# Kernel tuning notes

Measured on AMD Instinct MI355X. Metric: run time of the kernel, lower is better.

The kernel has to match this reference:

```python
import jax, jax.numpy as jnp
import numpy as np

EPS = 1e-12  # torch F.normalize eps


def _l2norm(x, axis):
    n = jnp.maximum(jnp.linalg.norm(x, axis=axis, keepdims=True), EPS)
    return x / n


def setup_inputs() -> dict:
    key = jax.random.key(0)
    k1, k2, k3, k4, k5 = jax.random.split(key, 5)
    N, E, IN_DIM, FAC_K, DIM_K = 100000, 1600000, 64, 4, 16
    all_emb = jax.random.normal(k1, (N, IN_DIM), dtype=jnp.float32) * 0.1
    W = jax.random.normal(k2, (FAC_K, IN_DIM, DIM_K), dtype=jnp.float32) * (1.0 / np.sqrt(IN_DIM))
    b = jax.random.normal(k3, (FAC_K, 1, DIM_K), dtype=jnp.float32) * 0.02
    row = jax.random.randint(k4, (E,), 0, N, dtype=jnp.int32)
    col = jax.random.randint(k5, (E,), 0, N, dtype=jnp.int32)
    return {"all_emb": all_emb, "W": W, "b": b, "row": row, "col": col, "iter_k": 2}


def reference(all_emb, W, b, row, col, iter_k):
    N = all_emb.shape[0]
    # factorized projection: [N, in_dim] x [K, in_dim, dk] -> [K, N, dk]
    fac = jnp.einsum('nd,kdf->knf', all_emb, W + b)
    fac = jax.nn.leaky_relu(fac, negative_slope=0.2)
    fac = _l2norm(fac, axis=2)

    new_fac = fac
    for _ in range(iter_k):
        head = new_fac[:, row]            # [K, E, dk]
        tail = fac[:, col]                # [K, E, dk]
        p_uv = jnp.sum(head * tail, axis=2)   # [K, E]
        p_uv = jax.nn.softmax(p_uv, axis=0)   # softmax over factors
        p_uv = jax.lax.stop_gradient(p_uv)    # original detaches attention
        msg = p_uv[:, :, None] * tail         # [K, E, dk]
        agg = jax.vmap(lambda m: jax.ops.segment_sum(m, row, num_segments=N))(msg)
        new_fac = _l2norm(fac + agg, axis=2)  # [K, N, dk]

    # torch.cat(list(new_fac_emb), dim=1) -> [N, K*dk]
    out = jnp.transpose(new_fac, (1, 0, 2)).reshape(N, -1)
    return out
```

## Files before the change

kernel.cpp:

```cpp
#include <hip/hip_runtime.h>

#define IN_DIM 64
#define FAC_K  4
#define DIM_K  16
#define SH     5
#define EPB    8192
#define CAP    1536

typedef _Float16 h2v __attribute__((ext_vector_type(2)));
typedef _Float16 h8v __attribute__((ext_vector_type(8)));
typedef float    f4v __attribute__((ext_vector_type(4)));

__device__ inline int   h2i(h2v v) { return __builtin_bit_cast(int, v); }
__device__ inline h2v   i2h(int v) { return __builtin_bit_cast(h2v, v); }
__device__ inline h2v   pkh(float a, float b) {
    return __builtin_bit_cast(h2v, __builtin_amdgcn_cvt_pkrtz(a, b));
}

#if __has_builtin(__builtin_amdgcn_fdot2)
__device__ inline float FDOT2(h2v a, h2v b, float c) {
    return __builtin_amdgcn_fdot2(a, b, c, false);
}
#else
__device__ inline float FDOT2(h2v a, h2v b, float c) {
    return c + (float)a.x * (float)b.x + (float)a.y * (float)b.y;
}
#endif

__device__ inline float qadd_xor1(float x) {
    int y = __builtin_amdgcn_update_dpp(0, __builtin_bit_cast(int, x), 0xB1, 0xF, 0xF, true);
    return x + __builtin_bit_cast(float, y);
}
__device__ inline float qadd_xor2(float x) {
    int y = __builtin_amdgcn_update_dpp(0, __builtin_bit_cast(int, x), 0x4E, 0xF, 0xF, true);
    return x + __builtin_bit_cast(float, y);
}
__device__ inline int rowxor8_i(int x) {
    return __builtin_amdgcn_update_dpp(0, x, 0x128, 0xF, 0xF, true);
}

union H8U { h8v v; h2v p[4]; };

#define TSZ 1344

__global__ __launch_bounds__(256) void fac_hist_kernel(
    const float* __restrict__ emb, const float* __restrict__ W,
    const float* __restrict__ b,   _Float16* __restrict__ fac16,
    const int* __restrict__ row,   int* __restrict__ H,
    int N, int E, int FB, int NB_blk, int NBUK)
{
    __shared__ float lds_pool[4 * TSZ];
    const int tid = threadIdx.x;

    if (blockIdx.x >= FB) {
        int* hist = (int*)lds_pool;
        const int hb   = blockIdx.x - FB;
        const int base = hb * EPB;
        for (int i = tid; i < NBUK; i += 256) hist[i] = 0;
        __syncthreads();
#pragma unroll
        for (int i = 0; i < EPB / 256; ++i) {
            int e = base + i * 256 + tid;
            if (e < E) atomicAdd(&hist[row[e] >> SH], 1);
        }
        __syncthreads();
        for (int i = tid; i < NBUK; i += 256)
            H[(size_t)i * NB_blk + hb] = hist[i];
        return;
    }

    const int lane = tid & 63;
    const int l    = lane & 15;
    const int q    = lane >> 4;
    float* T = lds_pool + (tid >> 6) * TSZ;

    H8U Bf[4][2];
#pragma unroll
    for (int t = 0; t < 4; ++t) {
        const float bv = b[16 * t + l];
#pragma unroll
        for (int s = 0; s < 2; ++s) {
            const float* wp = W + t * 1024 + (32 * s + 8 * q) * 16 + l;
#pragma unroll
            for (int jp = 0; jp < 4; ++jp) {
                float w0 = wp[(2 * jp)     * 16] + bv;
                float w1 = wp[(2 * jp + 1) * 16] + bv;
                Bf[t][s].p[jp] = pkh(w0, w1);
            }
        }
    }

    const int ntiles = (N + 15) >> 4;
    const int nw     = FB * 4;
    const int wid    = (blockIdx.x * 256 + tid) >> 6;

    for (int tile = wid; tile < ntiles; tile += nw) {
        const int n0 = tile << 4;
        int nm = n0 + l; if (nm >= N) nm = N - 1;

        f4v acc[4];
#pragma unroll
        for (int t = 0; t < 4; ++t) acc[t] = f4v{0.f, 0.f, 0.f, 0.f};

#pragma unroll
        for (int s = 0; s < 2; ++s) {
            const float4* ap = (const float4*)(emb + (size_t)nm * 64 + 32 * s + 8 * q);
            float4 a0 = ap[0], a1 = ap[1];
            H8U A;
            A.p[0] = pkh(a0.x, a0.y); A.p[1] = pkh(a0.z, a0.w);
            A.p[2] = pkh(a1.x, a1.y); A.p[3] = pkh(a1.z, a1.w);
#pragma unroll
            for (int t = 0; t < 4; ++t)
                acc[t] = __builtin_amdgcn_mfma_f32_16x16x32_f16(A.v, Bf[t][s].v, acc[t], 0, 0, 0);
        }

#pragma unroll
        for (int t = 0; t < 4; ++t) {
            f4v v = acc[t];
            f4v vr;
#pragma unroll
            for (int r = 0; r < 4; ++r)
                vr[r] = fmaxf(v[r], 0.f) + 0.2f * fminf(v[r], 0.f);
            const int o = 16 * t + l;
            ((f4v*)(T + 20 * o + 16 * t + 4 * q))[0] = vr;
        }
        float vv[16];
        float ss = 0.f;
#pragma unroll
        for (int i = 0; i < 16; ++i) {
            float x = T[20 * (16 * q + i) + 16 * q + l];
            vv[i] = x;
            ss = fmaf(x, x, ss);
        }
        float inv = 1.0f / fmaxf(sqrtf(ss), 1e-12f);
        H8U o0, o1;
#pragma unroll
        for (int jp = 0; jp < 4; ++jp) {
            o0.p[jp] = pkh(vv[2 * jp]     * inv, vv[2 * jp + 1] * inv);
            o1.p[jp] = pkh(vv[8 + 2 * jp] * inv, vv[9 + 2 * jp] * inv);
        }
        if (n0 + l < N) {
            uint4* dst = (uint4*)(fac16 + (size_t)(n0 + l) * 64 + q * 16);
            dst[0] = __builtin_bit_cast(uint4, o0.v);
            dst[1] = __builtin_bit_cast(uint4, o1.v);
        }
    }
}

__global__ __launch_bounds__(1024) void scan1_kernel(
    const int* __restrict__ in, int* __restrict__ out,
    int* __restrict__ bsum, int M)
{
    __shared__ int wsum[16];
    const int tid  = threadIdx.x;
    const int lane = tid & 63;
    const int w    = tid >> 6;
    const int gi   = blockIdx.x * 1024 + tid;

    int sc = (gi < M) ? in[gi] : 0;
#pragma unroll
    for (int d = 1; d < 64; d <<= 1) {
        int y = __shfl_up(sc, d);
        if (lane >= d) sc += y;
    }
    if (lane == 63) wsum[w] = sc;
    __syncthreads();
    if (w == 0) {
        int v = (lane < 16) ? wsum[lane] : 0;
#pragma unroll
        for (int d = 1; d < 16; d <<= 1) {
            int y = __shfl_up(v, d);
            if (lane >= d) v += y;
        }
        if (lane < 16) wsum[lane] = v;
    }
    __syncthreads();
    if (w > 0) sc += wsum[w - 1];
    if (gi < M) out[gi + 1] = sc;
    if (tid == 1023) bsum[blockIdx.x] = sc;
    if (blockIdx.x == 0 && tid == 0) out[0] = 0;
}

__global__ __launch_bounds__(1024) void scan2_kernel(int* __restrict__ bsum, int nb)
{
    __shared__ int sm[1024];
    const int tid = threadIdx.x;
    sm[tid] = (tid < nb) ? bsum[tid] : 0;
    __syncthreads();
    for (int d = 1; d < 1024; d <<= 1) {
        int t = (tid >= d) ? sm[tid - d] : 0;
        __syncthreads();
        sm[tid] += t;
        __syncthreads();
    }
    if (tid < nb) bsum[tid] = (tid > 0) ? sm[tid - 1] : 0;
}

__global__ __launch_bounds__(256) void scatter1_kernel(
    const int* __restrict__ row, const int* __restrict__ col,
    const int* __restrict__ Hscan, const int* __restrict__ bsum,
    int* __restrict__ tmp, int E, int NB_blk, int NBUK)
{
    __shared__ int cur[3200];
    const int tid = threadIdx.x;
    const int jb  = blockIdx.x;
    const int base = jb * EPB;
    for (int i = tid; i < NBUK; i += 256) {
        int g = i * NB_blk + jb;
        int v = Hscan[g];
        if (g >= 1) v += bsum[(g - 1) >> 10];
        cur[i] = v;
    }
    __syncthreads();
#pragma unroll
    for (int it = 0; it < EPB / 256; ++it) {
        int e = base + it * 256 + tid;
        if (e < E) {
            int r = row[e];
            int pos = atomicAdd(&cur[r >> SH], 1);
            tmp[pos] = ((r & 31) << 24) | (col[e] << 7);
        }
    }
}

__global__ __launch_bounds__(256, 8) void agg_kernel(
    const _Float16* __restrict__ fac16, const int* __restrict__ tmp,
    const int* __restrict__ Hscan, const int* __restrict__ bsum,
    float* __restrict__ nf_out, int E, int NB_blk, int NBUK, int N)
{
    __shared__ int csr[CAP];
    __shared__ int hist[32];
    __shared__ int curx[32];
    __shared__ int offl[33];

    const int tid = threadIdx.x;
    const int b   = blockIdx.x;

    const int g0 = b * NB_blk;
    const int gE = g0 + NB_blk;
    const int start = Hscan[g0] + (g0 >= 1 ? bsum[(g0 - 1) >> 10] : 0);
    const int end   = Hscan[gE] + bsum[(gE - 1) >> 10];
    const int cnt   = end - start;
    const bool fits = (cnt <= CAP);

    if (tid < 32) hist[tid] = 0;
    __syncthreads();
    if (fits) {
        for (int i = tid; i < cnt; i += 256)
            atomicAdd(&hist[tmp[start + i] >> 24], 1);
    }
    __syncthreads();
    if (tid < 32) {
        int e = hist[tid];
        int sc = e;
#pragma unroll
        for (int d = 1; d < 32; d <<= 1) {
            int y = __shfl_up(sc, d);
            if (tid >= d) sc += y;
        }
        int ex = sc - e;
        offl[tid] = ex;
        curx[tid] = ex;
        if (tid == 31) offl[32] = sc;
    }
    __syncthreads();
    if (fits) {
        for (int i = tid; i < cnt; i += 256) {
            int u = tmp[start + i];
            int pos = atomicAdd(&curx[u >> 24], 1);
            csr[pos] = u & 0xFFFFFF;
        }
    }
    __syncthreads();

    const int grp = tid >> 4;
    const int k   = tid & 3;
    const int q   = (tid >> 2) & 3;
    const char* facB = (const char*)fac16;
    const int   kb   = k * 32;

    for (int round = 0; round < 2; ++round) {
        const int lr = round * 16 + grp;
        const int n  = (b << SH) + lr;
        if (n >= N) continue;

        const _Float16* frow = fac16 + (size_t)n * 64 + k * 16;
        uint4 fa = ((const uint4*)frow)[0];
        uint4 fb = ((const uint4*)frow)[1];
        h2v fh[8] = { i2h(fa.x), i2h(fa.y), i2h(fa.z), i2h(fa.w),
                      i2h(fb.x), i2h(fb.y), i2h(fb.z), i2h(fb.w) };
        float f32[16];
#pragma unroll
        for (int r = 0; r < 8; ++r) { f32[2*r] = (float)fh[r].x; f32[2*r+1] = (float)fh[r].y; }
        h2v hh[8];
#pragma unroll
        for (int r = 0; r < 8; ++r) hh[r] = fh[r];

        int s_l = 0, len = 0;
        if (fits) { s_l = offl[lr]; len = offl[lr + 1] - s_l; }

        float vv[16];
#pragma unroll 1
        for (int pass = 0; pass < 2; ++pass) {
            h2v acc2[8];
#pragma unroll
            for (int r = 0; r < 8; ++r) acc2[r] = h2v{(_Float16)0.f, (_Float16)0.f};

            if (fits) {
                if (len > 0) {
                    int e0 = (q < len) ? q : len - 1;
                    const uint4* tp0 = (const uint4*)(facB + csr[s_l + e0] + kb);
                    uint4 ta0 = tp0[0], tb0 = tp0[1];
                    uint4 ta1 = ta0, tb1 = tb0;
                    if (len > 4) {
                        int e1 = (4 + q < len) ? 4 + q : len - 1;
                        const uint4* tp1 = (const uint4*)(facB + csr[s_l + e1] + kb);
                        ta1 = tp1[0]; tb1 = tp1[1];
                    }
                    for (int i = 0; i < len; i += 4) {
                        uint4 a = ta0, bb2 = tb0;
                        ta0 = ta1; tb0 = tb1;
                        const bool valid = (i + q) < len;
                        if (i + 8 < len) {
                            int e2 = (i + 8 + q < len) ? i + 8 + q : len - 1;
                            const uint4* tp2 = (const uint4*)(facB + csr[s_l + e2] + kb);
                            ta1 = tp2[0]; tb1 = tp2[1];
                        }
                        h2v t2[8] = { i2h(a.x), i2h(a.y), i2h(a.z), i2h(a.w),
                                      i2h(bb2.x), i2h(bb2.y), i2h(bb2.z), i2h(bb2.w) };
                        float p = 0.f;
#pragma unroll
                        for (int r = 0; r < 8; ++r) p = FDOT2(hh[r], t2[r], p);
                        float exv = valid ? __expf(p) : 0.f;
                        float qs = qadd_xor1(exv);
                        qs = qadd_xor2(qs);
                        float w = valid ? exv * __builtin_amdgcn_rcpf(qs) : 0.f;
                        _Float16 wh = (_Float16)w;
                        h2v w2; w2.x = wh; w2.y = wh;
#pragma unroll
                        for (int r = 0; r < 8; ++r) acc2[r] += w2 * t2[r];
                    }
                }
            } else {
                for (int i = 0; i < cnt; ++i) {
                    int u = tmp[start + i];
                    if ((u >> 24) != lr) continue;
                    const uint4* tp = (const uint4*)(facB + (u & 0xFFFFFF) + kb);
                    uint4 a = tp[0], bb2 = tp[1];
                    h2v t2[8] = { i2h(a.x), i2h(a.y), i2h(a.z), i2h(a.w),
                                  i2h(bb2.x), i2h(bb2.y), i2h(bb2.z), i2h(bb2.w) };
                    float p = 0.f;
#pragma unroll
                    for (int r = 0; r < 8; ++r) p = FDOT2(hh[r], t2[r], p);
                    float exv = __expf(p);
                    float qs = qadd_xor1(exv);
                    qs = qadd_xor2(qs);
                    float w = (q == 0) ? exv * __builtin_amdgcn_rcpf(qs) : 0.f;
                    _Float16 wh = (_Float16)w;
                    h2v w2; w2.x = wh; w2.y = wh;
#pragma unroll
                    for (int r = 0; r < 8; ++r) acc2[r] += w2 * t2[r];
                }
            }

#pragma unroll
            for (int r = 0; r < 8; ++r) {
                acc2[r] += i2h(__shfl_xor(h2i(acc2[r]), 4));
                acc2[r] += i2h(rowxor8_i(h2i(acc2[r])));
            }
            float ss = 0.f;
#pragma unroll
            for (int r = 0; r < 8; ++r) {
                vv[2*r]   = f32[2*r]   + (float)acc2[r].x;
                vv[2*r+1] = f32[2*r+1] + (float)acc2[r].y;
            }
#pragma unroll
            for (int d = 0; d < 16; ++d) ss = fmaf(vv[d], vv[d], ss);
            float inv = 1.0f / fmaxf(sqrtf(ss), 1e-12f);
#pragma unroll
            for (int d = 0; d < 16; ++d) vv[d] *= inv;
            if (pass == 0) {
#pragma unroll
                for (int r = 0; r < 8; ++r) {
                    h2v t; t.x = (_Float16)vv[2*r]; t.y = (_Float16)vv[2*r+1];
                    hh[r] = t;
                }
            }
        }

        float4 o;
        o.x = (q==0) ? vv[0]  : (q==1) ? vv[4]  : (q==2) ? vv[8]  : vv[12];
        o.y = (q==0) ? vv[1]  : (q==1) ? vv[5]  : (q==2) ? vv[9]  : vv[13];
        o.z = (q==0) ? vv[2]  : (q==1) ? vv[6]  : (q==2) ? vv[10] : vv[14];
        o.w = (q==0) ? vv[3]  : (q==1) ? vv[7]  : (q==2) ? vv[11] : vv[15];
        ((float4*)(nf_out + (size_t)n * 64 + k * 16))[q] = o;
    }
}

extern "C" void kernel_launch(void* const* d_in, const int* in_sizes, int n_in,
                              void* d_out, int out_size, void* d_ws, size_t ws_size,
                              hipStream_t stream) {
    const float* emb = (const float*)d_in[0];
    const float* W   = (const float*)d_in[1];
    const float* b   = (const float*)d_in[2];
    const int*   row = (const int*)d_in[3];
    const int*   col = (const int*)d_in[4];

    const int N = in_sizes[0] / IN_DIM;
    const int E = in_sizes[3];

    const int NBUK   = (N + 31) >> SH;
    const int NB_blk = (E + EPB - 1) / EPB;
    const int M      = NBUK * NB_blk;

    float* nf = (float*)d_out;

    _Float16* fac16 = (_Float16*)d_ws;
    int*      tmp   = (int*)(fac16 + (size_t)N * 64);
    int*      H     = tmp + E;
    int*      Hscan = H + M;
    int*      bsum  = Hscan + (M + 1);

    const int nb1 = (M + 1023) / 1024;
    const int FB  = 512;

    fac_hist_kernel<<<FB + NB_blk, 256, 0, stream>>>(
        emb, W, b, fac16, row, H, N, E, FB, NB_blk, NBUK);
    scan1_kernel<<<nb1, 1024, 0, stream>>>(H, Hscan, bsum, M);
    scan2_kernel<<<1, 1024, 0, stream>>>(bsum, nb1);
    scatter1_kernel<<<NB_blk, 256, 0, stream>>>(row, col, Hscan, bsum, tmp, E, NB_blk, NBUK);
    agg_kernel<<<NBUK, 256, 0, stream>>>(fac16, tmp, Hscan, bsum, nf, E, NB_blk, NBUK, N);
}
```

Before: 210.6 us.

## Replace per-block histogram scan with global bucket counts and atomic scatter

The per-(bucket, block) histogram matrix and its two-level scan are replaced by a single global per-bucket histogram built with global atomics, a one-block scan, and a scatter that claims positions through padded global atomic cursors. The aggregation kernel becomes persistent, with 2048 blocks pulling buckets from an atomic ticket counter. This cuts scan work and kernel launches, but adds contention on global atomics during the scatter and changes the order of edges inside each bucket, which also makes the fp16 accumulation order nondeterministic. The scan kernel handles at most 4096 buckets, which covers the 3125 buckets this input needs.

```diff
diff --git a/kernel.cpp b/kernel.cpp
--- a/kernel.cpp
+++ b/kernel.cpp
@@ -4,8 +4,8 @@
 #define FAC_K  4
 #define DIM_K  16
 #define SH     5
-#define EPB    8192
 #define CAP    1536
+#define HB     64
 
 typedef _Float16 h2v __attribute__((ext_vector_type(2)));
 typedef _Float16 h8v __attribute__((ext_vector_type(8)));
@@ -41,31 +41,35 @@
 
 union H8U { h8v v; h2v p[4]; };
 
+__global__ __launch_bounds__(256) void zero_kernel(int* __restrict__ p, int n)
+{
+    int i = blockIdx.x * 256 + threadIdx.x;
+    if (i < n) p[i] = 0;
+}
+
 #define TSZ 1344
 
 __global__ __launch_bounds__(256) void fac_hist_kernel(
     const float* __restrict__ emb, const float* __restrict__ W,
     const float* __restrict__ b,   _Float16* __restrict__ fac16,
-    const int* __restrict__ row,   int* __restrict__ H,
-    int N, int E, int FB, int NB_blk, int NBUK)
+    const int* __restrict__ row,   int* __restrict__ Hglob,
+    int N, int E, int FB, int NBUK)
 {
     __shared__ float lds_pool[4 * TSZ];
     const int tid = threadIdx.x;
 
     if (blockIdx.x >= FB) {
         int* hist = (int*)lds_pool;
-        const int hb   = blockIdx.x - FB;
-        const int base = hb * EPB;
+        const int hb = blockIdx.x - FB;
         for (int i = tid; i < NBUK; i += 256) hist[i] = 0;
         __syncthreads();
-#pragma unroll
-        for (int i = 0; i < EPB / 256; ++i) {
-            int e = base + i * 256 + tid;
-            if (e < E) atomicAdd(&hist[row[e] >> SH], 1);
-        }
-        __syncthreads();
-        for (int i = tid; i < NBUK; i += 256)
-            H[(size_t)i * NB_blk + hb] = hist[i];
+        for (int e = hb * 256 + tid; e < E; e += HB * 256)
+            atomicAdd(&hist[row[e] >> SH], 1);
+        __syncthreads();
+        for (int i = tid; i < NBUK; i += 256) {
+            int v = hist[i];
+            if (v) atomicAdd(&Hglob[i], v);
+        }
         return;
     }
 
@@ -147,17 +151,23 @@
     }
 }
 
-__global__ __launch_bounds__(1024) void scan1_kernel(
-    const int* __restrict__ in, int* __restrict__ out,
-    int* __restrict__ bsum, int M)
+__global__ __launch_bounds__(1024) void scan_kernel(
+    const int* __restrict__ Hglob, int* __restrict__ Hstart,
+    int* __restrict__ curp, int NBUK, int E)
 {
     __shared__ int wsum[16];
     const int tid  = threadIdx.x;
     const int lane = tid & 63;
     const int w    = tid >> 6;
-    const int gi   = blockIdx.x * 1024 + tid;
-
-    int sc = (gi < M) ? in[gi] : 0;
+    const int base = tid * 4;
+
+    int v[4]; int tot = 0;
+#pragma unroll
+    for (int j = 0; j < 4; ++j) {
+        v[j] = (base + j < NBUK) ? Hglob[base + j] : 0;
+        tot += v[j];
+    }
+    int sc = tot;
 #pragma unroll
     for (int d = 1; d < 64; d <<= 1) {
         int y = __shfl_up(sc, d);
@@ -166,234 +176,214 @@
     if (lane == 63) wsum[w] = sc;
     __syncthreads();
     if (w == 0) {
-        int v = (lane < 16) ? wsum[lane] : 0;
+        int t = (lane < 16) ? wsum[lane] : 0;
 #pragma unroll
         for (int d = 1; d < 16; d <<= 1) {
-            int y = __shfl_up(v, d);
-            if (lane >= d) v += y;
-        }
-        if (lane < 16) wsum[lane] = v;
+            int y = __shfl_up(t, d);
+            if (lane >= d) t += y;
+        }
+        if (lane < 16) wsum[lane] = t;
     }
     __syncthreads();
     if (w > 0) sc += wsum[w - 1];
-    if (gi < M) out[gi + 1] = sc;
-    if (tid == 1023) bsum[blockIdx.x] = sc;
-    if (blockIdx.x == 0 && tid == 0) out[0] = 0;
-}
-
-__global__ __launch_bounds__(1024) void scan2_kernel(int* __restrict__ bsum, int nb)
+    int run = sc - tot;
+#pragma unroll
+    for (int j = 0; j < 4; ++j) {
+        if (base + j < NBUK) {
+            Hstart[base + j] = run;
+            curp[(base + j) << 4] = run;
+        }
+        run += v[j];
+    }
+    if (tid == 0) Hstart[NBUK] = E;
+}
+
+__global__ __launch_bounds__(256) void scatter_kernel(
+    const int* __restrict__ row, const int* __restrict__ col,
+    int* __restrict__ curp, int* __restrict__ tmp, int E)
 {
-    __shared__ int sm[1024];
-    const int tid = threadIdx.x;
-    sm[tid] = (tid < nb) ? bsum[tid] : 0;
-    __syncthreads();
-    for (int d = 1; d < 1024; d <<= 1) {
-        int t = (tid >= d) ? sm[tid - d] : 0;
-        __syncthreads();
-        sm[tid] += t;
-        __syncthreads();
-    }
-    if (tid < nb) bsum[tid] = (tid > 0) ? sm[tid - 1] : 0;
-}
-
-__global__ __launch_bounds__(256) void scatter1_kernel(
-    const int* __restrict__ row, const int* __restrict__ col,
-    const int* __restrict__ Hscan, const int* __restrict__ bsum,
-    int* __restrict__ tmp, int E, int NB_blk, int NBUK)
-{
-    __shared__ int cur[3200];
-    const int tid = threadIdx.x;
-    const int jb  = blockIdx.x;
-    const int base = jb * EPB;
-    for (int i = tid; i < NBUK; i += 256) {
-        int g = i * NB_blk + jb;
-        int v = Hscan[g];
-        if (g >= 1) v += bsum[(g - 1) >> 10];
-        cur[i] = v;
-    }
-    __syncthreads();
-#pragma unroll
-    for (int it = 0; it < EPB / 256; ++it) {
-        int e = base + it * 256 + tid;
-        if (e < E) {
-            int r = row[e];
-            int pos = atomicAdd(&cur[r >> SH], 1);
-            tmp[pos] = ((r & 31) << 24) | (col[e] << 7);
-        }
+    int e = blockIdx.x * 256 + threadIdx.x;
+    if (e < E) {
+        int r = row[e];
+        int pos = atomicAdd(&curp[(r >> SH) << 4], 1);
+        tmp[pos] = ((r & 31) << 24) | (col[e] << 7);
     }
 }
 
 __global__ __launch_bounds__(256, 8) void agg_kernel(
     const _Float16* __restrict__ fac16, const int* __restrict__ tmp,
-    const int* __restrict__ Hscan, const int* __restrict__ bsum,
-    float* __restrict__ nf_out, int E, int NB_blk, int NBUK, int N)
+    const int* __restrict__ Hstart, int* __restrict__ tick,
+    float* __restrict__ nf_out, int NBUK, int N)
 {
     __shared__ int csr[CAP];
     __shared__ int hist[32];
     __shared__ int curx[32];
     __shared__ int offl[33];
+    __shared__ int sb;
 
     const int tid = threadIdx.x;
-    const int b   = blockIdx.x;
-
-    const int g0 = b * NB_blk;
-    const int gE = g0 + NB_blk;
-    const int start = Hscan[g0] + (g0 >= 1 ? bsum[(g0 - 1) >> 10] : 0);
-    const int end   = Hscan[gE] + bsum[(gE - 1) >> 10];
-    const int cnt   = end - start;
-    const bool fits = (cnt <= CAP);
-
-    if (tid < 32) hist[tid] = 0;
-    __syncthreads();
-    if (fits) {
-        for (int i = tid; i < cnt; i += 256)
-            atomicAdd(&hist[tmp[start + i] >> 24], 1);
-    }
-    __syncthreads();
-    if (tid < 32) {
-        int e = hist[tid];
-        int sc = e;
-#pragma unroll
-        for (int d = 1; d < 32; d <<= 1) {
-            int y = __shfl_up(sc, d);
-            if (tid >= d) sc += y;
-        }
-        int ex = sc - e;
-        offl[tid] = ex;
-        curx[tid] = ex;
-        if (tid == 31) offl[32] = sc;
-    }
-    __syncthreads();
-    if (fits) {
-        for (int i = tid; i < cnt; i += 256) {
-            int u = tmp[start + i];
-            int pos = atomicAdd(&curx[u >> 24], 1);
-            csr[pos] = u & 0xFFFFFF;
-        }
-    }
-    __syncthreads();
-
     const int grp = tid >> 4;
     const int k   = tid & 3;
     const int q   = (tid >> 2) & 3;
     const char* facB = (const char*)fac16;
     const int   kb   = k * 32;
 
-    for (int round = 0; round < 2; ++round) {
-        const int lr = round * 16 + grp;
-        const int n  = (b << SH) + lr;
-        if (n >= N) continue;
-
-        const _Float16* frow = fac16 + (size_t)n * 64 + k * 16;
-        uint4 fa = ((const uint4*)frow)[0];
-        uint4 fb = ((const uint4*)frow)[1];
-        h2v fh[8] = { i2h(fa.x), i2h(fa.y), i2h(fa.z), i2h(fa.w),
-                      i2h(fb.x), i2h(fb.y), i2h(fb.z), i2h(fb.w) };
-        float f32[16];
-#pragma unroll
-        for (int r = 0; r < 8; ++r) { f32[2*r] = (float)fh[r].x; f32[2*r+1] = (float)fh[r].y; }
-        h2v hh[8];
-#pragma unroll
-        for (int r = 0; r < 8; ++r) hh[r] = fh[r];
-
-        int s_l = 0, len = 0;
-        if (fits) { s_l = offl[lr]; len = offl[lr + 1] - s_l; }
-
-        float vv[16];
+    for (;;) {
+        if (tid == 0) sb = atomicAdd(tick, 1);
+        if (tid < 32) hist[tid] = 0;
+        __syncthreads();
+        const int b = sb;
+        if (b >= NBUK) break;
+
+        const int start = Hstart[b];
+        const int end   = Hstart[b + 1];
+        const int cnt   = end - start;
+        const bool fits = (cnt <= CAP);
+
+        if (fits) {
+            for (int i = tid; i < cnt; i += 256)
+                atomicAdd(&hist[tmp[start + i] >> 24], 1);
+        }
+        __syncthreads();
+        if (tid < 32) {
+            int e = hist[tid];
+            int sc = e;
+#pragma unroll
+            for (int d = 1; d < 32; d <<= 1) {
+                int y = __shfl_up(sc, d);
+                if (tid >= d) sc += y;
+            }
+            int ex = sc - e;
+            offl[tid] = ex;
+            curx[tid] = ex;
+            if (tid == 31) offl[32] = sc;
+        }
+        __syncthreads();
+        if (fits) {
+            for (int i = tid; i < cnt; i += 256) {
+                int u = tmp[start + i];
+                int pos = atomicAdd(&curx[u >> 24], 1);
+                csr[pos] = u & 0xFFFFFF;
+            }
+        }
+        __syncthreads();
+
+        for (int round = 0; round < 2; ++round) {
+            const int lr = round * 16 + grp;
+            const int n  = (b << SH) + lr;
+            if (n >= N) continue;
+
+            const _Float16* frow = fac16 + (size_t)n * 64 + k * 16;
+            uint4 fa = ((const uint4*)frow)[0];
+            uint4 fb = ((const uint4*)frow)[1];
+            h2v fh[8] = { i2h(fa.x), i2h(fa.y), i2h(fa.z), i2h(fa.w),
+                          i2h(fb.x), i2h(fb.y), i2h(fb.z), i2h(fb.w) };
+            float f32[16];
+#pragma unroll
+            for (int r = 0; r < 8; ++r) { f32[2*r] = (float)fh[r].x; f32[2*r+1] = (float)fh[r].y; }
+            h2v hh[8];
+#pragma unroll
+            for (int r = 0; r < 8; ++r) hh[r] = fh[r];
+
+            int s_l = 0, len = 0;
+            if (fits) { s_l = offl[lr]; len = offl[lr + 1] - s_l; }
+
+            float vv[16];
 #pragma unroll 1
-        for (int pass = 0; pass < 2; ++pass) {
-            h2v acc2[8];
-#pragma unroll
-            for (int r = 0; r < 8; ++r) acc2[r] = h2v{(_Float16)0.f, (_Float16)0.f};
-
-            if (fits) {
-                if (len > 0) {
-                    int e0 = (q < len) ? q : len - 1;
-                    const uint4* tp0 = (const uint4*)(facB + csr[s_l + e0] + kb);
-                    uint4 ta0 = tp0[0], tb0 = tp0[1];
-                    uint4 ta1 = ta0, tb1 = tb0;
-                    if (len > 4) {
-                        int e1 = (4 + q < len) ? 4 + q : len - 1;
-                        const uint4* tp1 = (const uint4*)(facB + csr[s_l + e1] + kb);
-                        ta1 = tp1[0]; tb1 = tp1[1];
+            for (int pass = 0; pass < 2; ++pass) {
+                h2v acc2[8];
+#pragma unroll
+                for (int r = 0; r < 8; ++r) acc2[r] = h2v{(_Float16)0.f, (_Float16)0.f};
+
+                if (fits) {
+                    if (len > 0) {
+                        int e0 = (q < len) ? q : len - 1;
+                        const uint4* tp0 = (const uint4*)(facB + csr[s_l + e0] + kb);
+                        uint4 ta0 = tp0[0], tb0 = tp0[1];
+                        uint4 ta1 = ta0, tb1 = tb0;
+                        if (len > 4) {
+                            int e1 = (4 + q < len) ? 4 + q : len - 1;
+                            const uint4* tp1 = (const uint4*)(facB + csr[s_l + e1] + kb);
+                            ta1 = tp1[0]; tb1 = tp1[1];
+                        }
+                        for (int i = 0; i < len; i += 4) {
+                            uint4 a = ta0, bb2 = tb0;
+                            ta0 = ta1; tb0 = tb1;
+                            const bool valid = (i + q) < len;
+                            if (i + 8 < len) {
+                                int e2 = (i + 8 + q < len) ? i + 8 + q : len - 1;
+                                const uint4* tp2 = (const uint4*)(facB + csr[s_l + e2] + kb);
+                                ta1 = tp2[0]; tb1 = tp2[1];
+                            }
+                            h2v t2[8] = { i2h(a.x), i2h(a.y), i2h(a.z), i2h(a.w),
+                                          i2h(bb2.x), i2h(bb2.y), i2h(bb2.z), i2h(bb2.w) };
+                            float p = 0.f;
+#pragma unroll
+                            for (int r = 0; r < 8; ++r) p = FDOT2(hh[r], t2[r], p);
+                            float exv = valid ? __expf(p) : 0.f;
+                            float qs = qadd_xor1(exv);
+                            qs = qadd_xor2(qs);
+                            float w = valid ? exv * __builtin_amdgcn_rcpf(qs) : 0.f;
+                            _Float16 wh = (_Float16)w;
+                            h2v w2; w2.x = wh; w2.y = wh;
+#pragma unroll
+                            for (int r = 0; r < 8; ++r) acc2[r] += w2 * t2[r];
+                        }
                     }
-                    for (int i = 0; i < len; i += 4) {
-                        uint4 a = ta0, bb2 = tb0;
-                        ta0 = ta1; tb0 = tb1;
-                        const bool valid = (i + q) < len;
-                        if (i + 8 < len) {
-                            int e2 = (i + 8 + q < len) ? i + 8 + q : len - 1;
-                            const uint4* tp2 = (const uint4*)(facB + csr[s_l + e2] + kb);
-                            ta1 = tp2[0]; tb1 = tp2[1];
-                        }
+                } else {
+                    for (int i = 0; i < cnt; ++i) {
+                        int u = tmp[start + i];
+                        if ((u >> 24) != lr) continue;
+                        const uint4* tp = (const uint4*)(facB + (u & 0xFFFFFF) + kb);
+                        uint4 a = tp[0], bb2 = tp[1];
                         h2v t2[8] = { i2h(a.x), i2h(a.y), i2h(a.z), i2h(a.w),
                                       i2h(bb2.x), i2h(bb2.y), i2h(bb2.z), i2h(bb2.w) };
                         float p = 0.f;
 #pragma unroll
                         for (int r = 0; r < 8; ++r) p = FDOT2(hh[r], t2[r], p);
-                        float exv = valid ? __expf(p) : 0.f;
+                        float exv = __expf(p);
                         float qs = qadd_xor1(exv);
                         qs = qadd_xor2(qs);
-                        float w = valid ? exv * __builtin_amdgcn_rcpf(qs) : 0.f;
+                        float w = (q == 0) ? exv * __builtin_amdgcn_rcpf(qs) : 0.f;
                         _Float16 wh = (_Float16)w;
                         h2v w2; w2.x = wh; w2.y = wh;
 #pragma unroll
                         for (int r = 0; r < 8; ++r) acc2[r] += w2 * t2[r];
                     }
                 }
-            } else {
-                for (int i = 0; i < cnt; ++i) {
-                    int u = tmp[start + i];
-                    if ((u >> 24) != lr) continue;
-                    const uint4* tp = (const uint4*)(facB + (u & 0xFFFFFF) + kb);
-                    uint4 a = tp[0], bb2 = tp[1];
-                    h2v t2[8] = { i2h(a.x), i2h(a.y), i2h(a.z), i2h(a.w),
-                                  i2h(bb2.x), i2h(bb2.y), i2h(bb2.z), i2h(bb2.w) };
-                    float p = 0.f;
-#pragma unroll
-                    for (int r = 0; r < 8; ++r) p = FDOT2(hh[r], t2[r], p);
-                    float exv = __expf(p);
-                    float qs = qadd_xor1(exv);
-                    qs = qadd_xor2(qs);
-                    float w = (q == 0) ? exv * __builtin_amdgcn_rcpf(qs) : 0.f;
-                    _Float16 wh = (_Float16)w;
-                    h2v w2; w2.x = wh; w2.y = wh;
-#pragma unroll
-                    for (int r = 0; r < 8; ++r) acc2[r] += w2 * t2[r];
+
+#pragma unroll
+                for (int r = 0; r < 8; ++r) {
+                    acc2[r] += i2h(__shfl_xor(h2i(acc2[r]), 4));
+                    acc2[r] += i2h(rowxor8_i(h2i(acc2[r])));
+                }
+                float ss = 0.f;
+#pragma unroll
+                for (int r = 0; r < 8; ++r) {
+                    vv[2*r]   = f32[2*r]   + (float)acc2[r].x;
+                    vv[2*r+1] = f32[2*r+1] + (float)acc2[r].y;
+                }
+#pragma unroll
+                for (int d = 0; d < 16; ++d) ss = fmaf(vv[d], vv[d], ss);
+                float inv = 1.0f / fmaxf(sqrtf(ss), 1e-12f);
+#pragma unroll
+                for (int d = 0; d < 16; ++d) vv[d] *= inv;
+                if (pass == 0) {
+#pragma unroll
+                    for (int r = 0; r < 8; ++r) {
+                        h2v t; t.x = (_Float16)vv[2*r]; t.y = (_Float16)vv[2*r+1];
+                        hh[r] = t;
+                    }
                 }
             }
 
-#pragma unroll
-            for (int r = 0; r < 8; ++r) {
-                acc2[r] += i2h(__shfl_xor(h2i(acc2[r]), 4));
-                acc2[r] += i2h(rowxor8_i(h2i(acc2[r])));
-            }
-            float ss = 0.f;
-#pragma unroll
-            for (int r = 0; r < 8; ++r) {
-                vv[2*r]   = f32[2*r]   + (float)acc2[r].x;
-                vv[2*r+1] = f32[2*r+1] + (float)acc2[r].y;
-            }
-#pragma unroll
-            for (int d = 0; d < 16; ++d) ss = fmaf(vv[d], vv[d], ss);
-            float inv = 1.0f / fmaxf(sqrtf(ss), 1e-12f);
-#pragma unroll
-            for (int d = 0; d < 16; ++d) vv[d] *= inv;
-            if (pass == 0) {
-#pragma unroll
-                for (int r = 0; r < 8; ++r) {
-                    h2v t; t.x = (_Float16)vv[2*r]; t.y = (_Float16)vv[2*r+1];
-                    hh[r] = t;
-                }
-            }
-        }
-
-        float4 o;
-        o.x = (q==0) ? vv[0]  : (q==1) ? vv[4]  : (q==2) ? vv[8]  : vv[12];
-        o.y = (q==0) ? vv[1]  : (q==1) ? vv[5]  : (q==2) ? vv[9]  : vv[13];
-        o.z = (q==0) ? vv[2]  : (q==1) ? vv[6]  : (q==2) ? vv[10] : vv[14];
-        o.w = (q==0) ? vv[3]  : (q==1) ? vv[7]  : (q==2) ? vv[11] : vv[15];
-        ((float4*)(nf_out + (size_t)n * 64 + k * 16))[q] = o;
+            float4 o;
+            o.x = (q==0) ? vv[0]  : (q==1) ? vv[4]  : (q==2) ? vv[8]  : vv[12];
+            o.y = (q==0) ? vv[1]  : (q==1) ? vv[5]  : (q==2) ? vv[9]  : vv[13];
+            o.z = (q==0) ? vv[2]  : (q==1) ? vv[6]  : (q==2) ? vv[10] : vv[14];
+            o.w = (q==0) ? vv[3]  : (q==1) ? vv[7]  : (q==2) ? vv[11] : vv[15];
+            ((float4*)(nf_out + (size_t)n * 64 + k * 16))[q] = o;
+        }
     }
 }
 
@@ -409,25 +399,23 @@
     const int N = in_sizes[0] / IN_DIM;
     const int E = in_sizes[3];
 
-    const int NBUK   = (N + 31) >> SH;
-    const int NB_blk = (E + EPB - 1) / EPB;
-    const int M      = NBUK * NB_blk;
+    const int NBUK = (N + 31) >> SH;
 
     float* nf = (float*)d_out;
 
-    _Float16* fac16 = (_Float16*)d_ws;
-    int*      tmp   = (int*)(fac16 + (size_t)N * 64);
-    int*      H     = tmp + E;
-    int*      Hscan = H + M;
-    int*      bsum  = Hscan + (M + 1);
-
-    const int nb1 = (M + 1023) / 1024;
-    const int FB  = 512;
-
-    fac_hist_kernel<<<FB + NB_blk, 256, 0, stream>>>(
-        emb, W, b, fac16, row, H, N, E, FB, NB_blk, NBUK);
-    scan1_kernel<<<nb1, 1024, 0, stream>>>(H, Hscan, bsum, M);
-    scan2_kernel<<<1, 1024, 0, stream>>>(bsum, nb1);
-    scatter1_kernel<<<NB_blk, 256, 0, stream>>>(row, col, Hscan, bsum, tmp, E, NB_blk, NBUK);
-    agg_kernel<<<NBUK, 256, 0, stream>>>(fac16, tmp, Hscan, bsum, nf, E, NB_blk, NBUK, N);
-}
+    _Float16* fac16  = (_Float16*)d_ws;
+    int*      tmp    = (int*)(fac16 + (size_t)N * 64);
+    int*      Hglob  = tmp + E;
+    int*      tick   = Hglob + NBUK;
+    int*      Hstart = tick + 1;
+    int*      curp   = Hstart + NBUK + 1;
+
+    const int FB = 512;
+
+    zero_kernel<<<(NBUK + 1 + 255) / 256, 256, 0, stream>>>(Hglob, NBUK + 1);
+    fac_hist_kernel<<<FB + HB, 256, 0, stream>>>(
+        emb, W, b, fac16, row, Hglob, N, E, FB, NBUK);
+    scan_kernel<<<1, 1024, 0, stream>>>(Hglob, Hstart, curp, NBUK, E);
+    scatter_kernel<<<(E + 255) / 256, 256, 0, stream>>>(row, col, curp, tmp, E);
+    agg_kernel<<<2048, 256, 0, stream>>>(fac16, tmp, Hstart, tick, nf, NBUK, N);
+}
```

New measurement: 349.3 us. 1.66x slower.

## Stage gathered tail rows in LDS for reuse in second aggregation pass

Applied to the files above, without the earlier changes.

In the first pass the agg kernel writes the gathered fp16 tail vectors for the first STG edges of each block into a shared-memory staging buffer, using a swizzled layout. The second pass then reads those edges from LDS and gathers only the remaining edges from global memory. This is meant to cut repeated random global gathers. It costs 32KB of extra LDS, and the occupancy hint is lowered from 8 to 4 blocks per SM.

```diff
diff --git a/kernel.cpp b/kernel.cpp
--- a/kernel.cpp
+++ b/kernel.cpp
@@ -6,6 +6,7 @@
 #define SH     5
 #define EPB    8192
 #define CAP    1536
+#define STG    256
 
 typedef _Float16 h2v __attribute__((ext_vector_type(2)));
 typedef _Float16 h8v __attribute__((ext_vector_type(8)));
@@ -223,12 +224,13 @@
     }
 }
 
-__global__ __launch_bounds__(256, 8) void agg_kernel(
+__global__ __launch_bounds__(256, 4) void agg_kernel(
     const _Float16* __restrict__ fac16, const int* __restrict__ tmp,
     const int* __restrict__ Hscan, const int* __restrict__ bsum,
     float* __restrict__ nf_out, int E, int NB_blk, int NBUK, int N)
 {
     __shared__ int csr[CAP];
+    __shared__ uint4 stage[STG * 8];
     __shared__ int hist[32];
     __shared__ int curx[32];
     __shared__ int offl[33];
@@ -298,6 +300,12 @@
 
         int s_l = 0, len = 0;
         if (fits) { s_l = offl[lr]; len = offl[lr + 1] - s_l; }
+        int nl = 0;
+        {
+            int t = STG - s_l;
+            nl = (t < 0) ? 0 : (t > len ? len : t);
+            nl &= ~3;
+        }
 
         float vv[16];
 #pragma unroll 1
@@ -307,7 +315,7 @@
             for (int r = 0; r < 8; ++r) acc2[r] = h2v{(_Float16)0.f, (_Float16)0.f};
 
             if (fits) {
-                if (len > 0) {
+                if (pass == 0 && len > 0) {
                     int e0 = (q < len) ? q : len - 1;
                     const uint4* tp0 = (const uint4*)(facB + csr[s_l + e0] + kb);
                     uint4 ta0 = tp0[0], tb0 = tp0[1];
@@ -326,6 +334,13 @@
                             const uint4* tp2 = (const uint4*)(facB + csr[s_l + e2] + kb);
                             ta1 = tp2[0]; tb1 = tp2[1];
                         }
+                        if (valid) {
+                            int g = s_l + i + q;
+                            if (g < STG) {
+                                int u = (g << 3) + (((k + g) & 3) << 1);
+                                stage[u] = a; stage[u + 1] = bb2;
+                            }
+                        }
                         h2v t2[8] = { i2h(a.x), i2h(a.y), i2h(a.z), i2h(a.w),
                                       i2h(bb2.x), i2h(bb2.y), i2h(bb2.z), i2h(bb2.w) };
                         float p = 0.f;
@@ -339,6 +354,61 @@
                         h2v w2; w2.x = wh; w2.y = wh;
 #pragma unroll
                         for (int r = 0; r < 8; ++r) acc2[r] += w2 * t2[r];
+                    }
+                } else if (pass == 1 && len > 0) {
+                    for (int i = 0; i < nl; i += 4) {
+                        int g = s_l + i + q;
+                        int u = (g << 3) + (((k + g) & 3) << 1);
+                        uint4 a = stage[u], bb2 = stage[u + 1];
+                        h2v t2[8] = { i2h(a.x), i2h(a.y), i2h(a.z), i2h(a.w),
+                                      i2h(bb2.x), i2h(bb2.y), i2h(bb2.z), i2h(bb2.w) };
+                        float p = 0.f;
+#pragma unroll
+                        for (int r = 0; r < 8; ++r) p = FDOT2(hh[r], t2[r], p);
+                        float exv = __expf(p);
+                        float qs = qadd_xor1(exv);
+                        qs = qadd_xor2(qs);
+                        float w = exv * __builtin_amdgcn_rcpf(qs);
+                        _Float16 wh = (_Float16)w;
+                        h2v w2; w2.x = wh; w2.y = wh;
+#pragma unroll
+                        for (int r = 0; r < 8; ++r) acc2[r] += w2 * t2[r];
+                    }
+                    const int s_l2 = s_l + nl;
+                    const int len2 = len - nl;
+                    if (len2 > 0) {
+                        int e0 = (q < len2) ? q : len2 - 1;
+                        const uint4* tp0 = (const uint4*)(facB + csr[s_l2 + e0] + kb);
+                        uint4 ta0 = tp0[0], tb0 = tp0[1];
+                        uint4 ta1 = ta0, tb1 = tb0;
+                        if (len2 > 4) {
+                            int e1 = (4 + q < len2) ? 4 + q : len2 - 1;
+                            const uint4* tp1 = (const uint4*)(facB + csr[s_l2 + e1] + kb);
+                            ta1 = tp1[0]; tb1 = tp1[1];
+                        }
+                        for (int i = 0; i < len2; i += 4) {
+                            uint4 a = ta0, bb2 = tb0;
+                            ta0 = ta1; tb0 = tb1;
+                            const bool valid = (i + q) < len2;
+                            if (i + 8 < len2) {
+                                int e2 = (i + 8 + q < len2) ? i + 8 + q : len2 - 1;
+                                const uint4* tp2 = (const uint4*)(facB + csr[s_l2 + e2] + kb);
+                                ta1 = tp2[0]; tb1 = tp2[1];
+                            }
+                            h2v t2[8] = { i2h(a.x), i2h(a.y), i2h(a.z), i2h(a.w),
+                                          i2h(bb2.x), i2h(bb2.y), i2h(bb2.z), i2h(bb2.w) };
+                            float p = 0.f;
+#pragma unroll
+                            for (int r = 0; r < 8; ++r) p = FDOT2(hh[r], t2[r], p);
+                            float exv = valid ? __expf(p) : 0.f;
+                            float qs = qadd_xor1(exv);
+                            qs = qadd_xor2(qs);
+                            float w = valid ? exv * __builtin_amdgcn_rcpf(qs) : 0.f;
+                            _Float16 wh = (_Float16)w;
+                            h2v w2; w2.x = wh; w2.y = wh;
+#pragma unroll
+                            for (int r = 0; r < 8; ++r) acc2[r] += w2 * t2[r];
+                        }
                     }
                 }
             } else {
```

New measurement: 203.4 us. 1.04x faster.
